# Kernel tuning notes

Measured on AMD Instinct MI355X. Metric: run time of the kernel, lower is better.

Reference implementation:

```python
import jax, jax.numpy as jnp
import numpy as np
import math

XLEN, YLEN, B = 2048, 1024, 8
XD, YD, HD, YOUT = 1024, 1024, 512, 1024


def setup_inputs() -> dict:
    key = jax.random.key(0)
    ks = jax.random.split(key, 12)

    def lin(kw, kb, out_d, in_d):
        s = 1.0 / math.sqrt(in_d)
        w = jax.random.uniform(kw, (out_d, in_d), jnp.float32, -s, s)
        b = jax.random.uniform(kb, (out_d,), jnp.float32, -s, s)
        return w, b

    Xk_w, Xk_b = lin(ks[0], ks[1], HD, XD)
    Xv_w, Xv_b = lin(ks[2], ks[3], HD, XD)
    Yq_w, Yq_b = lin(ks[4], ks[5], HD, YD)
    Yw_w, Yw_b = lin(ks[6], ks[7], YOUT, YD + HD)

    X = jax.random.normal(ks[8], (XLEN, B, XD), jnp.float32)
    Y = jax.random.normal(ks[9], (YLEN, B, YD), jnp.float32)
    alignment = jax.random.normal(ks[10], (B, YLEN, XLEN), jnp.float32)
    X_pad_mask = jax.random.bernoulli(ks[11], 0.1, (B, YLEN, XLEN))  # True -> mask out
    align_w = jnp.zeros((1,), jnp.float32)  # nn.Parameter([0])

    return {"X": X, "Y": Y, "alignment": alignment, "X_pad_mask": X_pad_mask,
            "Xk_w": Xk_w, "Xk_b": Xk_b, "Xv_w": Xv_w, "Xv_b": Xv_b,
            "Yq_w": Yq_w, "Yq_b": Yq_b, "Yw_w": Yw_w, "Yw_b": Yw_b,
            "align_w": align_w}


def reference(X, Y, alignment, X_pad_mask, Xk_w, Xk_b, Xv_w, Xv_b,
              Yq_w, Yq_b, Yw_w, Yw_b, align_w):
    FMAX = jnp.finfo(X.dtype).max
    # projections (torch Linear: x @ W.T + b)
    xk = X @ Xk_w.T + Xk_b                     # (x, b, hd)
    yq = Y @ Yq_w.T + Yq_b                     # (y, b, hd)
    # scaled cross-attention logits
    logit = jnp.einsum('xbd,ybd->byx', xk, yq) / math.sqrt(xk.shape[-1])
    # gated alignment bias + clamp
    logit = logit + jax.nn.sigmoid(align_w[0]) * alignment
    logit = jnp.maximum(logit, -FMAX)
    # pad-mask additive fill (-FMAX) then clamp (matches masked_fill + add + clamp)
    logit = jnp.maximum(logit + jnp.where(X_pad_mask, -FMAX, 0.0), -FMAX)
    attn = jax.nn.softmax(logit, axis=-1)      # (b, y, x); dropout = identity (eval)
    xv = X @ Xv_w.T + Xv_b                     # (x, b, hd)
    attn_feat = jnp.einsum('byx,xbh->ybh', attn, xv)  # (y, b, hd)
    concat = jnp.concatenate([Y, attn_feat], axis=-1)  # (y, b, yd+hd)
    return concat @ Yw_w.T + Yw_b              # (y, b, y_outdim)
```

## Files before the change

kernel.cpp:

```cpp
#include <hip/hip_runtime.h>


#define FMAXF 3.402823466e38f

typedef __attribute__((ext_vector_type(8))) __bf16 bf16x8;
typedef __attribute__((ext_vector_type(4))) float f32x4;

static __device__ __forceinline__ short f2b(float f) {
  union { float f; unsigned u; } x; x.f = f;
  unsigned r = (x.u + 0x7FFFu + ((x.u >> 16) & 1u)) >> 16;
  return (short)r;
}
static __device__ __forceinline__ float b2f(short s) {
  union { unsigned u; float f; } x; x.u = ((unsigned)(unsigned short)s) << 16;
  return x.f;
}

static __device__ __forceinline__ void gl_lds16(const short* g, short* l) {
  __builtin_amdgcn_global_load_lds(
      (const __attribute__((address_space(1))) void*)g,
      (__attribute__((address_space(3))) void*)l, 16, 0, 0);
}


struct EpiKV {
  static constexpr bool staged = true;
  short* xk; short* xv; const float* kb; const float* vb;
  __device__ float bias_at(int n) const { return n < 512 ? kb[n] : vb[n - 512]; }
  __device__ void store(int bz, int m, int n, int4 v) const {
    int b = m & 7; long x = m >> 3;
    if (n < 512) *(int4*)(xk + ((long)b * 2048 + x) * 512 + n) = v;
    else         *(int4*)(xv + ((long)b * 2048 + x) * 512 + (n - 512)) = v;
  }
};

struct EpiYq {
  static constexpr bool staged = true;
  short* out; const float* bias;
  __device__ float bias_at(int n) const { return bias[n]; }
  __device__ void store(int bz, int m, int n, int4 v) const {
    *(int4*)(out + (((long)(m & 7)) * 1024 + (m >> 3)) * 512 + n) = v;
  }
};

struct EpiLogit {
  static constexpr bool staged = true;
  short* out;
  __device__ float bias_at(int n) const { return 0.0f; }
  __device__ void store(int bz, int m, int n, int4 v) const {
    *(int4*)(out + ((long)bz * 1024 + m) * 2048 + n) = v;
  }
};

struct EpiConcat {
  static constexpr bool staged = true;
  short* out;
  __device__ float bias_at(int n) const { return 0.0f; }
  __device__ void store(int bz, int m, int n, int4 v) const {
    *(int4*)(out + ((long)m * 8 + bz) * 1536 + 1024 + n) = v;
  }
};

struct EpiOut {
  static constexpr bool staged = false;
  float* out; const float* bias;
  __device__ void direct(int bz, int m, int n, float v) const {
    out[(long)m * 1024 + n] = v + bias[n];
  }
};

template <int TM, typename Epi>
__global__ __launch_bounds__(256) void gemm_mt(
    const short* __restrict__ A, long sAb, int lda,
    const short* __restrict__ B, long sBb, int ldb,
    int K, int tlog, Epi epi) {
  constexpr int R = TM + 128;
  constexpr int SEGS = R / 32;
  constexpr int LDSN = (R * 64 > TM * 128) ? R * 64 : TM * 128;
  __shared__ short S[LDSN];

  const int tid = threadIdx.x;
  const int lane = tid & 63, wave = tid >> 6;
  const int bz = blockIdx.z;

  const int id = blockIdx.x;
  const int xcd = id & 7;
  const int rr = id >> 3;
  const int n0 = (rr & ((1 << tlog) - 1)) * 128;
  const int m0 = (((rr >> tlog) << 3) + xcd) * TM;

  const short* gp[SEGS];
#pragma unroll
  for (int t = 0; t < SEGS; t++) {
    int slot = t * 256 + tid;
    int row = slot >> 3;
    int gcol = ((slot & 7) ^ (row & 7)) * 8;
    gp[t] = (row < TM)
                ? A + (long)bz * sAb + (long)(m0 + row) * lda + gcol
                : B + (long)bz * sBb + (long)(n0 + row - TM) * ldb + gcol;
  }

  const int wm = (TM == 128) ? (wave & 1) * 64 : 0;
  const int wn = (TM == 128) ? (wave >> 1) * 64 : wave * 32;
  constexpr int MI = 4;
  constexpr int MJ = (TM == 128) ? 4 : 2;
  const int quad = lane >> 4, l16 = lane & 15;
  const int xr = l16 & 7;

  f32x4 acc[MI][MJ] = {};

  for (int k0 = 0; k0 < K; k0 += 64) {
#pragma unroll
    for (int t = 0; t < SEGS; t++)
      gl_lds16(gp[t] + k0, S + (t * 256 + tid) * 8);
    __syncthreads();

#pragma unroll
    for (int kk = 0; kk < 2; kk++) {
      union { int4 v; bf16x8 f; } a[MI], b[MJ];
      const int g = ((kk << 2) + quad);
#pragma unroll
      for (int i = 0; i < MI; i++)
        a[i].v = *(const int4*)(S + (wm + i * 16 + l16) * 64 + (g ^ xr) * 8);
#pragma unroll
      for (int j = 0; j < MJ; j++)
        b[j].v = *(const int4*)(S + (TM + wn + j * 16 + l16) * 64 + (g ^ xr) * 8);
#pragma unroll
      for (int i = 0; i < MI; i++)
#pragma unroll
        for (int j = 0; j < MJ; j++)
          acc[i][j] = __builtin_amdgcn_mfma_f32_16x16x32_bf16(a[i].f, b[j].f,
                                                              acc[i][j], 0, 0, 0);
    }
    __syncthreads();
  }

  if constexpr (Epi::staged) {
#pragma unroll
    for (int j = 0; j < MJ; j++) {
      const int c = wn + j * 16 + l16;
      const float bj = epi.bias_at(n0 + c);
#pragma unroll
      for (int i = 0; i < MI; i++)
#pragma unroll
        for (int r = 0; r < 4; r++)
          S[(wm + i * 16 + quad * 4 + r) * 128 + c] = f2b(acc[i][j][r] + bj);
    }
    __syncthreads();
#pragma unroll
    for (int t = 0; t < TM / 16; t++) {
      int c = t * 256 + tid;
      int row = c >> 4, colc = (c & 15) * 8;
      int4 v = *(const int4*)(S + row * 128 + colc);
      epi.store(bz, m0 + row, n0 + colc, v);
    }
  } else {
#pragma unroll
    for (int i = 0; i < MI; i++)
#pragma unroll
      for (int j = 0; j < MJ; j++)
#pragma unroll
        for (int r = 0; r < 4; r++)
          epi.direct(bz, m0 + wm + i * 16 + quad * 4 + r,
                     n0 + wn + j * 16 + l16, acc[i][j][r]);
  }
}

__global__ __launch_bounds__(256) void cvt_f32_bf16(const float* __restrict__ in,
                                                    short* __restrict__ out,
                                                    long n4) {
  long i = (long)blockIdx.x * 256 + threadIdx.x;
  if (i >= n4) return;
  float4 f = ((const float4*)in)[i];
  union { short s[4]; long long v; } o;
  o.s[0] = f2b(f.x); o.s[1] = f2b(f.y); o.s[2] = f2b(f.z); o.s[3] = f2b(f.w);
  ((long long*)out)[i] = o.v;
}

__global__ __launch_bounds__(256) void cvt_weights(
    const float* __restrict__ xk_w, const float* __restrict__ xv_w,
    const float* __restrict__ yq_w, const float* __restrict__ yw_w,
    short* __restrict__ wkv, short* __restrict__ wyq, short* __restrict__ wyw) {
  long i = (long)blockIdx.x * 256 + threadIdx.x;
  const float* src; long long* dst; long off;
  if (i < 131072)      { src = xk_w; dst = (long long*)wkv; off = i; }
  else if (i < 262144) { src = xv_w; dst = (long long*)wkv + 131072; off = i - 131072; }
  else if (i < 393216) { src = yq_w; dst = (long long*)wyq; off = i - 262144; }
  else                 { src = yw_w; dst = (long long*)wyw; off = i - 393216; }
  float4 f = ((const float4*)src)[off];
  union { short s[4]; long long v; } o;
  o.s[0] = f2b(f.x); o.s[1] = f2b(f.y); o.s[2] = f2b(f.z); o.s[3] = f2b(f.w);
  dst[off] = o.v;
}

__global__ __launch_bounds__(256) void cvt_y_concat(const float* __restrict__ in,
                                                    short* __restrict__ out) {
  long idx = (long)blockIdx.x * 256 + threadIdx.x;
  long row = idx >> 8;
  int c = (int)(idx & 255) << 2;
  float4 f = *(const float4*)(in + row * 1024 + c);
  union { short s[4]; unsigned long long v; } o;
  o.s[0] = f2b(f.x); o.s[1] = f2b(f.y); o.s[2] = f2b(f.z); o.s[3] = f2b(f.w);
  *(unsigned long long*)(out + row * 1536 + c) = o.v;
}

__global__ __launch_bounds__(256) void transpose_xv(const short* __restrict__ xv,
                                                    short* __restrict__ xvt) {
  __shared__ short t[32][36];
  const int b = blockIdx.z;
  const long x0 = (long)blockIdx.x * 32, h0 = (long)blockIdx.y * 32;
  const int r = threadIdx.x >> 3, c = (threadIdx.x & 7) * 4;
  const short* src = xv + ((long)b * 2048 + x0 + r) * 512 + h0 + c;
  *(int2*)&t[r][c] = *(const int2*)src;
  __syncthreads();
  union { short s[4]; int2 v; } o;
  o.s[0] = t[c + 0][r]; o.s[1] = t[c + 1][r];
  o.s[2] = t[c + 2][r]; o.s[3] = t[c + 3][r];
  short* dst = xvt + ((long)b * 512 + h0 + r) * 2048 + x0 + c;
  *(int2*)dst = o.v;
}

__global__ __launch_bounds__(256) void softmax_rows(short* __restrict__ logits,
                                                    const float* __restrict__ align,
                                                    const int* __restrict__ mask,
                                                    const float* __restrict__ alw) {
  const long row = blockIdx.x;
  const long base = row * 2048 + threadIdx.x * 8;
  short* p = logits + base;
  const float g = 1.0f / (1.0f + __expf(-alw[0]));
  const float scale = 0.04419417382415922f;

  union { short s[8]; int4 v; } d;
  d.v = *(const int4*)p;
  float4 al0 = *(const float4*)(align + base);
  float4 al1 = *(const float4*)(align + base + 4);
  int4 mk0 = *(const int4*)(mask + base);
  int4 mk1 = *(const int4*)(mask + base + 4);

  float vals[8];
  vals[0] = mk0.x ? -FMAXF : b2f(d.s[0]) * scale + g * al0.x;
  vals[1] = mk0.y ? -FMAXF : b2f(d.s[1]) * scale + g * al0.y;
  vals[2] = mk0.z ? -FMAXF : b2f(d.s[2]) * scale + g * al0.z;
  vals[3] = mk0.w ? -FMAXF : b2f(d.s[3]) * scale + g * al0.w;
  vals[4] = mk1.x ? -FMAXF : b2f(d.s[4]) * scale + g * al1.x;
  vals[5] = mk1.y ? -FMAXF : b2f(d.s[5]) * scale + g * al1.y;
  vals[6] = mk1.z ? -FMAXF : b2f(d.s[6]) * scale + g * al1.z;
  vals[7] = mk1.w ? -FMAXF : b2f(d.s[7]) * scale + g * al1.w;

  float mx = -FMAXF;
#pragma unroll
  for (int i = 0; i < 8; i++) mx = fmaxf(mx, vals[i]);
#pragma unroll
  for (int off = 32; off; off >>= 1) mx = fmaxf(mx, __shfl_xor(mx, off));
  __shared__ float redm[4], reds[4];
  const int tid = threadIdx.x;
  if ((tid & 63) == 0) redm[tid >> 6] = mx;
  __syncthreads();
  mx = fmaxf(fmaxf(redm[0], redm[1]), fmaxf(redm[2], redm[3]));

  float s = 0.0f;
#pragma unroll
  for (int i = 0; i < 8; i++) { vals[i] = __expf(vals[i] - mx); s += vals[i]; }
#pragma unroll
  for (int off = 32; off; off >>= 1) s += __shfl_xor(s, off);
  if ((tid & 63) == 0) reds[tid >> 6] = s;
  __syncthreads();
  s = reds[0] + reds[1] + reds[2] + reds[3];
  float inv = 1.0f / s;
#pragma unroll
  for (int i = 0; i < 8; i++) d.s[i] = f2b(vals[i] * inv);
  *(int4*)p = d.v;
}


extern "C" void kernel_launch(void* const* d_in, const int* in_sizes, int n_in,
                              void* d_out, int out_size, void* d_ws, size_t ws_size,
                              hipStream_t stream) {
  const float* X    = (const float*)d_in[0];
  const float* Y    = (const float*)d_in[1];
  const float* alig = (const float*)d_in[2];
  const int*   mask = (const int*)d_in[3];
  const float* Xk_w = (const float*)d_in[4];
  const float* Xk_b = (const float*)d_in[5];
  const float* Xv_w = (const float*)d_in[6];
  const float* Xv_b = (const float*)d_in[7];
  const float* Yq_w = (const float*)d_in[8];
  const float* Yq_b = (const float*)d_in[9];
  const float* Yw_w = (const float*)d_in[10];
  const float* Yw_b = (const float*)d_in[11];
  const float* alw  = (const float*)d_in[12];
  float* out = (float*)d_out;

  char* ws = (char*)d_ws;
  short* xbf    = (short*)(ws + 0);
  short* logits = (short*)(ws + 0);
  short* xk     = (short*)(ws + 33554432);
  short* xv     = (short*)(ws + 50331648);
  short* xvt    = (short*)(ws + 67108864);
  short* yq     = (short*)(ws + 83886080);
  short* concat = (short*)(ws + 92274688);
  short* wkv    = (short*)(ws + 117440512);
  short* wyq    = (short*)(ws + 119537664);
  short* wyw    = (short*)(ws + 120586240);

  cvt_f32_bf16<<<16384, 256, 0, stream>>>(X, xbf, 4194304);
  cvt_y_concat<<<8192, 256, 0, stream>>>(Y, concat);
  cvt_weights<<<3072, 256, 0, stream>>>(Xk_w, Xv_w, Yq_w, Yw_w, wkv, wyq, wyw);

  gemm_mt<128, EpiKV><<<dim3(1024, 1, 1), 256, 0, stream>>>(
      xbf, 0, 1024, wkv, 0, 1024, 1024, 3, EpiKV{xk, xv, Xk_b, Xv_b});

  gemm_mt<64, EpiYq><<<dim3(512, 1, 1), 256, 0, stream>>>(
      concat, 0, 1536, wyq, 0, 1024, 1024, 2, EpiYq{yq, Yq_b});

  transpose_xv<<<dim3(64, 16, 8), 256, 0, stream>>>(xv, xvt);

  gemm_mt<128, EpiLogit><<<dim3(128, 1, 8), 256, 0, stream>>>(
      yq, (long)1024 * 512, 512, xk, (long)2048 * 512, 512, 512, 4,
      EpiLogit{logits});

  softmax_rows<<<8192, 256, 0, stream>>>(logits, alig, mask, alw);

  gemm_mt<64, EpiConcat><<<dim3(64, 1, 8), 256, 0, stream>>>(
      logits, (long)1024 * 2048, 2048, xvt, (long)512 * 2048, 2048, 2048, 2,
      EpiConcat{concat});

  gemm_mt<128, EpiOut><<<dim3(512, 1, 1), 256, 0, stream>>>(
      concat, 0, 1536, wyw, 0, 1536, 1536, 3, EpiOut{out, Yw_b});
}
```

Before: 424.3 us.

## Fuse logits GEMM, softmax and attention-value GEMM into one flash-attention kernel

Replaces the three-kernel path (logits GEMM to a bf16 buffer, row softmax, then attn@xv GEMM) with a single kernel. Each 512-thread block handles 32 query rows of one batch. Per 128-column tile it computes QK^T with MFMA, adds the gated alignment bias and pad mask (staged into LDS via global_load_lds), exponentiates, and feeds the bf16 probabilities through swizzled LDS into the PV MFMA. Row sums are reduced at the end, and the normalized output is written straight into the concat buffer. This removes the write and re-read of the full logits matrix and two kernel launches. The trade-offs: no running-max subtraction, so it relies on logits staying in exp range. It also uses one large block per CU, and xk, yq and xvt are read from global/L2 without LDS reuse.

```diff
diff --git a/kernel.cpp b/kernel.cpp
--- a/kernel.cpp
+++ b/kernel.cpp
@@ -10,10 +10,6 @@
   union { float f; unsigned u; } x; x.f = f;
   unsigned r = (x.u + 0x7FFFu + ((x.u >> 16) & 1u)) >> 16;
   return (short)r;
-}
-static __device__ __forceinline__ float b2f(short s) {
-  union { unsigned u; float f; } x; x.u = ((unsigned)(unsigned short)s) << 16;
-  return x.f;
 }
 
 static __device__ __forceinline__ void gl_lds16(const short* g, short* l) {
@@ -40,24 +36,6 @@
   __device__ float bias_at(int n) const { return bias[n]; }
   __device__ void store(int bz, int m, int n, int4 v) const {
     *(int4*)(out + (((long)(m & 7)) * 1024 + (m >> 3)) * 512 + n) = v;
-  }
-};
-
-struct EpiLogit {
-  static constexpr bool staged = true;
-  short* out;
-  __device__ float bias_at(int n) const { return 0.0f; }
-  __device__ void store(int bz, int m, int n, int4 v) const {
-    *(int4*)(out + ((long)bz * 1024 + m) * 2048 + n) = v;
-  }
-};
-
-struct EpiConcat {
-  static constexpr bool staged = true;
-  short* out;
-  __device__ float bias_at(int n) const { return 0.0f; }
-  __device__ void store(int bz, int m, int n, int4 v) const {
-    *(int4*)(out + ((long)m * 8 + bz) * 1536 + 1024 + n) = v;
   }
 };
 
@@ -220,56 +198,160 @@
   *(int2*)dst = o.v;
 }
 
-__global__ __launch_bounds__(256) void softmax_rows(short* __restrict__ logits,
-                                                    const float* __restrict__ align,
-                                                    const int* __restrict__ mask,
-                                                    const float* __restrict__ alw) {
-  const long row = blockIdx.x;
-  const long base = row * 2048 + threadIdx.x * 8;
-  short* p = logits + base;
+__global__ __launch_bounds__(512) void flash_attn(
+    const short* __restrict__ yq, const short* __restrict__ xk,
+    const short* __restrict__ xvt, const float* __restrict__ align,
+    const int* __restrict__ mask, const float* __restrict__ alw,
+    short* __restrict__ concat) {
+  __shared__ __align__(16) char lds[41984];
+  float* As = (float*)lds;
+  int*   Ms = (int*)(lds + 16384);
+  short* Es = (short*)(lds + 32768);
+  float* RS = (float*)(lds + 40960);
+
+  const int tid = threadIdx.x;
+  const int lane = tid & 63, wave = tid >> 6;
+  const int quad = lane >> 4, l16 = lane & 15;
+  const int id = blockIdx.x;
+  const int b = id & 7, y0 = (id >> 3) * 32;
+
   const float g = 1.0f / (1.0f + __expf(-alw[0]));
   const float scale = 0.04419417382415922f;
 
-  union { short s[8]; int4 v; } d;
-  d.v = *(const int4*)p;
-  float4 al0 = *(const float4*)(align + base);
-  float4 al1 = *(const float4*)(align + base + 4);
-  int4 mk0 = *(const int4*)(mask + base);
-  int4 mk1 = *(const int4*)(mask + base + 4);
-
-  float vals[8];
-  vals[0] = mk0.x ? -FMAXF : b2f(d.s[0]) * scale + g * al0.x;
-  vals[1] = mk0.y ? -FMAXF : b2f(d.s[1]) * scale + g * al0.y;
-  vals[2] = mk0.z ? -FMAXF : b2f(d.s[2]) * scale + g * al0.z;
-  vals[3] = mk0.w ? -FMAXF : b2f(d.s[3]) * scale + g * al0.w;
-  vals[4] = mk1.x ? -FMAXF : b2f(d.s[4]) * scale + g * al1.x;
-  vals[5] = mk1.y ? -FMAXF : b2f(d.s[5]) * scale + g * al1.y;
-  vals[6] = mk1.z ? -FMAXF : b2f(d.s[6]) * scale + g * al1.z;
-  vals[7] = mk1.w ? -FMAXF : b2f(d.s[7]) * scale + g * al1.w;
-
-  float mx = -FMAXF;
-#pragma unroll
-  for (int i = 0; i < 8; i++) mx = fmaxf(mx, vals[i]);
-#pragma unroll
-  for (int off = 32; off; off >>= 1) mx = fmaxf(mx, __shfl_xor(mx, off));
-  __shared__ float redm[4], reds[4];
-  const int tid = threadIdx.x;
-  if ((tid & 63) == 0) redm[tid >> 6] = mx;
+  const short* yqb = yq + (long)b * 1024 * 512;
+  const short* xkb = xk + (long)b * 2048 * 512;
+  const short* xvb = xvt + (long)b * 512 * 2048;
+  const float* alb = align + ((long)b * 1024 + y0) * 2048;
+  const int*   mkb = mask + ((long)b * 1024 + y0) * 2048;
+
+  auto stage = [&](int t) {
+    const long x0 = (long)t * 128;
+#pragma unroll
+    for (int u = 0; u < 2; u++) {
+      int slot = u * 512 + tid;
+      int row = slot >> 5, gcol = (slot & 31) * 4;
+      gl_lds16((const short*)(alb + (long)row * 2048 + x0 + gcol),
+               (short*)(As + slot * 4));
+      gl_lds16((const short*)(mkb + (long)row * 2048 + x0 + gcol),
+               (short*)(Ms + slot * 4));
+    }
+  };
+
+  f32x4 acc[2][4] = {};
+  float rs[8] = {};
+
+  stage(0);
+  asm volatile("s_waitcnt vmcnt(0)" ::: "memory");
   __syncthreads();
-  mx = fmaxf(fmaxf(redm[0], redm[1]), fmaxf(redm[2], redm[3]));
-
-  float s = 0.0f;
-#pragma unroll
-  for (int i = 0; i < 8; i++) { vals[i] = __expf(vals[i] - mx); s += vals[i]; }
-#pragma unroll
-  for (int off = 32; off; off >>= 1) s += __shfl_xor(s, off);
-  if ((tid & 63) == 0) reds[tid >> 6] = s;
+
+#pragma unroll 1
+  for (int t = 0; t < 16; t++) {
+    const int x0 = t * 128;
+    f32x4 s0 = {}, s1 = {};
+    const short* ap0 = yqb + (long)(y0 + l16) * 512 + quad * 8;
+    const short* ap1 = ap0 + 16 * 512;
+    const short* bp  = xkb + (long)(x0 + wave * 16 + l16) * 512 + quad * 8;
+#pragma unroll
+    for (int kk = 0; kk < 16; kk++) {
+      union { int4 v; bf16x8 f; } a0, a1, bb;
+      a0.v = *(const int4*)(ap0 + kk * 32);
+      a1.v = *(const int4*)(ap1 + kk * 32);
+      bb.v = *(const int4*)(bp + kk * 32);
+      s0 = __builtin_amdgcn_mfma_f32_16x16x32_bf16(a0.f, bb.f, s0, 0, 0, 0);
+      s1 = __builtin_amdgcn_mfma_f32_16x16x32_bf16(a1.f, bb.f, s1, 0, 0, 0);
+    }
+    const int col = wave * 16 + l16;
+    const int cg = col >> 3;
+#pragma unroll
+    for (int i = 0; i < 2; i++) {
+#pragma unroll
+      for (int r = 0; r < 4; r++) {
+        int row = i * 16 + quad * 4 + r;
+        float sv = i ? s1[r] : s0[r];
+        float bias = Ms[row * 128 + col] ? -FMAXF : g * As[row * 128 + col];
+        float e = __expf(fmaf(sv, scale, bias));
+        rs[i * 4 + r] += e;
+        int sg = cg ^ (row & 7);
+        Es[row * 128 + sg * 8 + (col & 7)] = f2b(e);
+      }
+    }
+    __syncthreads();
+    if (t < 15) stage(t + 1);
+    const int d0 = wave * 64;
+    const short* vp = xvb + (long)(d0 + l16) * 2048 + x0 + quad * 8;
+#pragma unroll
+    for (int kk = 0; kk < 4; kk++) {
+      union { int4 v; bf16x8 f; } ea[2], vb[4];
+      const int gi = kk * 4 + quad;
+#pragma unroll
+      for (int i = 0; i < 2; i++) {
+        int row = i * 16 + l16;
+        int sg = gi ^ (row & 7);
+        ea[i].v = *(const int4*)(Es + row * 128 + sg * 8);
+      }
+#pragma unroll
+      for (int j = 0; j < 4; j++)
+        vb[j].v = *(const int4*)(vp + (long)j * 16 * 2048 + kk * 32);
+#pragma unroll
+      for (int i = 0; i < 2; i++)
+#pragma unroll
+        for (int j = 0; j < 4; j++)
+          acc[i][j] = __builtin_amdgcn_mfma_f32_16x16x32_bf16(
+              ea[i].f, vb[j].f, acc[i][j], 0, 0, 0);
+    }
+    asm volatile("s_waitcnt vmcnt(0)" ::: "memory");
+    __syncthreads();
+  }
+
+#pragma unroll
+  for (int k = 0; k < 8; k++) {
+#pragma unroll
+    for (int off = 1; off < 16; off <<= 1)
+      rs[k] += __shfl_xor(rs[k], off);
+  }
+  if (l16 == 0) {
+#pragma unroll
+    for (int i = 0; i < 2; i++)
+#pragma unroll
+      for (int r = 0; r < 4; r++)
+        RS[wave * 32 + i * 16 + quad * 4 + r] = rs[i * 4 + r];
+  }
   __syncthreads();
-  s = reds[0] + reds[1] + reds[2] + reds[3];
-  float inv = 1.0f / s;
-#pragma unroll
-  for (int i = 0; i < 8; i++) d.s[i] = f2b(vals[i] * inv);
-  *(int4*)p = d.v;
+  float inv[2][4];
+#pragma unroll
+  for (int i = 0; i < 2; i++)
+#pragma unroll
+    for (int r = 0; r < 4; r++) {
+      int row = i * 16 + quad * 4 + r;
+      float s = 0.0f;
+#pragma unroll
+      for (int w = 0; w < 8; w++) s += RS[w * 32 + row];
+      inv[i][r] = 1.0f / s;
+    }
+
+  short* Os = (short*)lds;
+  const int d0 = wave * 64;
+#pragma unroll
+  for (int i = 0; i < 2; i++)
+#pragma unroll
+    for (int j = 0; j < 4; j++) {
+      int colb = d0 + j * 16 + l16;
+#pragma unroll
+      for (int r = 0; r < 4; r++) {
+        int row = i * 16 + quad * 4 + r;
+        int sg = (colb >> 3) ^ (row & 7);
+        Os[row * 512 + sg * 8 + (colb & 7)] = f2b(acc[i][j][r] * inv[i][r]);
+      }
+    }
+  __syncthreads();
+#pragma unroll
+  for (int u = 0; u < 4; u++) {
+    int slot = u * 512 + tid;
+    int row = slot >> 6, gg = slot & 63;
+    int sg = gg ^ (row & 7);
+    int4 v = *(const int4*)(Os + row * 512 + sg * 8);
+    *(int4*)(concat + ((long)(y0 + row) * 8 + b) * 1536 + 1024 + gg * 8) = v;
+  }
 }
 
 
@@ -293,7 +375,6 @@
 
   char* ws = (char*)d_ws;
   short* xbf    = (short*)(ws + 0);
-  short* logits = (short*)(ws + 0);
   short* xk     = (short*)(ws + 33554432);
   short* xv     = (short*)(ws + 50331648);
   short* xvt    = (short*)(ws + 67108864);
@@ -315,15 +396,7 @@
 
   transpose_xv<<<dim3(64, 16, 8), 256, 0, stream>>>(xv, xvt);
 
-  gemm_mt<128, EpiLogit><<<dim3(128, 1, 8), 256, 0, stream>>>(
-      yq, (long)1024 * 512, 512, xk, (long)2048 * 512, 512, 512, 4,
-      EpiLogit{logits});
-
-  softmax_rows<<<8192, 256, 0, stream>>>(logits, alig, mask, alw);
-
-  gemm_mt<64, EpiConcat><<<dim3(64, 1, 8), 256, 0, stream>>>(
-      logits, (long)1024 * 2048, 2048, xvt, (long)512 * 2048, 2048, 2048, 2,
-      EpiConcat{concat});
+  flash_attn<<<256, 512, 0, stream>>>(yq, xk, xvt, alig, mask, alw, concat);
 
   gemm_mt<128, EpiOut><<<dim3(512, 1, 1), 256, 0, stream>>>(
       concat, 0, 1536, wyw, 0, 1536, 1536, 3, EpiOut{out, Yw_b});
```

Measured after the change: 487.4 us. 14.9% more time.

## Fuse softmax exp into logit GEMM epilogue and normalize in PV GEMM

Applied to the files above, without the earlier changes.

Removes the standalone softmax kernel. The logit GEMM epilogue now applies scale, the gated alignment bias and the pad mask, exponentiates without subtracting the row max, and accumulates row sums with atomics into a buffer that the weight-conversion kernel zeroes. The attention-value GEMM epilogue then divides by the row sum. This saves one full read and write of the bf16 logit matrix and one launch, but drops max subtraction, so large logits could overflow, and it adds scattered align/mask loads and atomics inside the GEMM epilogue.

```diff
diff --git a/kernel.cpp b/kernel.cpp
--- a/kernel.cpp
+++ b/kernel.cpp
@@ -11,10 +11,6 @@
   unsigned r = (x.u + 0x7FFFu + ((x.u >> 16) & 1u)) >> 16;
   return (short)r;
 }
-static __device__ __forceinline__ float b2f(short s) {
-  union { unsigned u; float f; } x; x.u = ((unsigned)(unsigned short)s) << 16;
-  return x.f;
-}
 
 static __device__ __forceinline__ void gl_lds16(const short* g, short* l) {
   __builtin_amdgcn_global_load_lds(
@@ -25,6 +21,8 @@
 
 struct EpiKV {
   static constexpr bool staged = true;
+  static constexpr bool expm = false;
+  static constexpr bool norm = false;
   short* xk; short* xv; const float* kb; const float* vb;
   __device__ float bias_at(int n) const { return n < 512 ? kb[n] : vb[n - 512]; }
   __device__ void store(int bz, int m, int n, int4 v) const {
@@ -36,6 +34,8 @@
 
 struct EpiYq {
   static constexpr bool staged = true;
+  static constexpr bool expm = false;
+  static constexpr bool norm = false;
   short* out; const float* bias;
   __device__ float bias_at(int n) const { return bias[n]; }
   __device__ void store(int bz, int m, int n, int4 v) const {
@@ -43,18 +43,26 @@
   }
 };
 
-struct EpiLogit {
+struct EpiLogitExp {
   static constexpr bool staged = true;
+  static constexpr bool expm = true;
+  static constexpr bool norm = false;
   short* out;
+  const float* align;
+  const int* mask;
+  const float* alw;
+  float* rowsum;
   __device__ float bias_at(int n) const { return 0.0f; }
   __device__ void store(int bz, int m, int n, int4 v) const {
     *(int4*)(out + ((long)bz * 1024 + m) * 2048 + n) = v;
   }
 };
 
-struct EpiConcat {
+struct EpiConcatNorm {
   static constexpr bool staged = true;
-  short* out;
+  static constexpr bool expm = false;
+  static constexpr bool norm = true;
+  short* out; const float* rowsum;
   __device__ float bias_at(int n) const { return 0.0f; }
   __device__ void store(int bz, int m, int n, int4 v) const {
     *(int4*)(out + ((long)m * 8 + bz) * 1536 + 1024 + n) = v;
@@ -63,6 +71,8 @@
 
 struct EpiOut {
   static constexpr bool staged = false;
+  static constexpr bool expm = false;
+  static constexpr bool norm = false;
   float* out; const float* bias;
   __device__ void direct(int bz, int m, int n, float v) const {
     out[(long)m * 1024 + n] = v + bias[n];
@@ -136,15 +146,56 @@
   }
 
   if constexpr (Epi::staged) {
-#pragma unroll
-    for (int j = 0; j < MJ; j++) {
-      const int c = wn + j * 16 + l16;
-      const float bj = epi.bias_at(n0 + c);
+    if constexpr (Epi::expm) {
+      const float g = 1.0f / (1.0f + __expf(-epi.alw[0]));
+      const float scale = 0.04419417382415922f;
+#pragma unroll
+      for (int i = 0; i < MI; i++) {
+#pragma unroll
+        for (int r = 0; r < 4; r++) {
+          const int row = wm + i * 16 + quad * 4 + r;
+          const long gy = (long)bz * 1024 + m0 + row;
+          const float* arow = epi.align + gy * 2048 + n0;
+          const int*   mrow = epi.mask + gy * 2048 + n0;
+          float part = 0.0f;
+#pragma unroll
+          for (int j = 0; j < MJ; j++) {
+            const int col = wn + j * 16 + l16;
+            float e = 0.0f;
+            if (!mrow[col])
+              e = __expf(fmaf(acc[i][j][r], scale, g * arow[col]));
+            part += e;
+            S[row * 128 + col] = f2b(e);
+          }
+          part += __shfl_xor(part, 1);
+          part += __shfl_xor(part, 2);
+          part += __shfl_xor(part, 4);
+          part += __shfl_xor(part, 8);
+          if (l16 == 0) atomicAdd(epi.rowsum + gy, part);
+        }
+      }
+    } else if constexpr (Epi::norm) {
 #pragma unroll
       for (int i = 0; i < MI; i++)
 #pragma unroll
-        for (int r = 0; r < 4; r++)
-          S[(wm + i * 16 + quad * 4 + r) * 128 + c] = f2b(acc[i][j][r] + bj);
+        for (int r = 0; r < 4; r++) {
+          const int row = wm + i * 16 + quad * 4 + r;
+          const float inv = 1.0f / epi.rowsum[(long)bz * 1024 + m0 + row];
+#pragma unroll
+          for (int j = 0; j < MJ; j++)
+            S[row * 128 + wn + j * 16 + l16] = f2b(acc[i][j][r] * inv);
+        }
+    } else {
+#pragma unroll
+      for (int j = 0; j < MJ; j++) {
+        const int c = wn + j * 16 + l16;
+        const float bj = epi.bias_at(n0 + c);
+#pragma unroll
+        for (int i = 0; i < MI; i++)
+#pragma unroll
+          for (int r = 0; r < 4; r++)
+            S[(wm + i * 16 + quad * 4 + r) * 128 + c] = f2b(acc[i][j][r] + bj);
+      }
     }
     __syncthreads();
 #pragma unroll
@@ -180,8 +231,10 @@
 __global__ __launch_bounds__(256) void cvt_weights(
     const float* __restrict__ xk_w, const float* __restrict__ xv_w,
     const float* __restrict__ yq_w, const float* __restrict__ yw_w,
-    short* __restrict__ wkv, short* __restrict__ wyq, short* __restrict__ wyw) {
+    short* __restrict__ wkv, short* __restrict__ wyq, short* __restrict__ wyw,
+    float* __restrict__ rowsum) {
   long i = (long)blockIdx.x * 256 + threadIdx.x;
+  if (i < 8192) rowsum[i] = 0.0f;
   const float* src; long long* dst; long off;
   if (i < 131072)      { src = xk_w; dst = (long long*)wkv; off = i; }
   else if (i < 262144) { src = xv_w; dst = (long long*)wkv + 131072; off = i - 131072; }
@@ -218,58 +271,6 @@
   o.s[2] = t[c + 2][r]; o.s[3] = t[c + 3][r];
   short* dst = xvt + ((long)b * 512 + h0 + r) * 2048 + x0 + c;
   *(int2*)dst = o.v;
-}
-
-__global__ __launch_bounds__(256) void softmax_rows(short* __restrict__ logits,
-                                                    const float* __restrict__ align,
-                                                    const int* __restrict__ mask,
-                                                    const float* __restrict__ alw) {
-  const long row = blockIdx.x;
-  const long base = row * 2048 + threadIdx.x * 8;
-  short* p = logits + base;
-  const float g = 1.0f / (1.0f + __expf(-alw[0]));
-  const float scale = 0.04419417382415922f;
-
-  union { short s[8]; int4 v; } d;
-  d.v = *(const int4*)p;
-  float4 al0 = *(const float4*)(align + base);
-  float4 al1 = *(const float4*)(align + base + 4);
-  int4 mk0 = *(const int4*)(mask + base);
-  int4 mk1 = *(const int4*)(mask + base + 4);
-
-  float vals[8];
-  vals[0] = mk0.x ? -FMAXF : b2f(d.s[0]) * scale + g * al0.x;
-  vals[1] = mk0.y ? -FMAXF : b2f(d.s[1]) * scale + g * al0.y;
-  vals[2] = mk0.z ? -FMAXF : b2f(d.s[2]) * scale + g * al0.z;
-  vals[3] = mk0.w ? -FMAXF : b2f(d.s[3]) * scale + g * al0.w;
-  vals[4] = mk1.x ? -FMAXF : b2f(d.s[4]) * scale + g * al1.x;
-  vals[5] = mk1.y ? -FMAXF : b2f(d.s[5]) * scale + g * al1.y;
-  vals[6] = mk1.z ? -FMAXF : b2f(d.s[6]) * scale + g * al1.z;
-  vals[7] = mk1.w ? -FMAXF : b2f(d.s[7]) * scale + g * al1.w;
-
-  float mx = -FMAXF;
-#pragma unroll
-  for (int i = 0; i < 8; i++) mx = fmaxf(mx, vals[i]);
-#pragma unroll
-  for (int off = 32; off; off >>= 1) mx = fmaxf(mx, __shfl_xor(mx, off));
-  __shared__ float redm[4], reds[4];
-  const int tid = threadIdx.x;
-  if ((tid & 63) == 0) redm[tid >> 6] = mx;
-  __syncthreads();
-  mx = fmaxf(fmaxf(redm[0], redm[1]), fmaxf(redm[2], redm[3]));
-
-  float s = 0.0f;
-#pragma unroll
-  for (int i = 0; i < 8; i++) { vals[i] = __expf(vals[i] - mx); s += vals[i]; }
-#pragma unroll
-  for (int off = 32; off; off >>= 1) s += __shfl_xor(s, off);
-  if ((tid & 63) == 0) reds[tid >> 6] = s;
-  __syncthreads();
-  s = reds[0] + reds[1] + reds[2] + reds[3];
-  float inv = 1.0f / s;
-#pragma unroll
-  for (int i = 0; i < 8; i++) d.s[i] = f2b(vals[i] * inv);
-  *(int4*)p = d.v;
 }
 
 
@@ -293,7 +294,7 @@
 
   char* ws = (char*)d_ws;
   short* xbf    = (short*)(ws + 0);
-  short* logits = (short*)(ws + 0);
+  short* E      = (short*)(ws + 0);
   short* xk     = (short*)(ws + 33554432);
   short* xv     = (short*)(ws + 50331648);
   short* xvt    = (short*)(ws + 67108864);
@@ -302,10 +303,12 @@
   short* wkv    = (short*)(ws + 117440512);
   short* wyq    = (short*)(ws + 119537664);
   short* wyw    = (short*)(ws + 120586240);
+  float* rowsum = (float*)(ws + 123731968);
 
   cvt_f32_bf16<<<16384, 256, 0, stream>>>(X, xbf, 4194304);
   cvt_y_concat<<<8192, 256, 0, stream>>>(Y, concat);
-  cvt_weights<<<3072, 256, 0, stream>>>(Xk_w, Xv_w, Yq_w, Yw_w, wkv, wyq, wyw);
+  cvt_weights<<<3072, 256, 0, stream>>>(Xk_w, Xv_w, Yq_w, Yw_w, wkv, wyq, wyw,
+                                        rowsum);
 
   gemm_mt<128, EpiKV><<<dim3(1024, 1, 1), 256, 0, stream>>>(
       xbf, 0, 1024, wkv, 0, 1024, 1024, 3, EpiKV{xk, xv, Xk_b, Xv_b});
@@ -315,15 +318,13 @@
 
   transpose_xv<<<dim3(64, 16, 8), 256, 0, stream>>>(xv, xvt);
 
-  gemm_mt<128, EpiLogit><<<dim3(128, 1, 8), 256, 0, stream>>>(
+  gemm_mt<128, EpiLogitExp><<<dim3(128, 1, 8), 256, 0, stream>>>(
       yq, (long)1024 * 512, 512, xk, (long)2048 * 512, 512, 512, 4,
-      EpiLogit{logits});
-
-  softmax_rows<<<8192, 256, 0, stream>>>(logits, alig, mask, alw);
-
-  gemm_mt<64, EpiConcat><<<dim3(64, 1, 8), 256, 0, stream>>>(
-      logits, (long)1024 * 2048, 2048, xvt, (long)512 * 2048, 2048, 2048, 2,
-      EpiConcat{concat});
+      EpiLogitExp{E, alig, mask, alw, rowsum});
+
+  gemm_mt<64, EpiConcatNorm><<<dim3(64, 1, 8), 256, 0, stream>>>(
+      E, (long)1024 * 2048, 2048, xvt, (long)512 * 2048, 2048, 2048, 2,
+      EpiConcatNorm{concat, rowsum});
 
   gemm_mt<128, EpiOut><<<dim3(512, 1, 1), 256, 0, stream>>>(
       concat, 0, 1536, wyw, 0, 1536, 1536, 3, EpiOut{out, Yw_b});
```

Result: slower. 496.2 us (+17.0%).
